# Optimization experiments

Hardware: AMD Instinct MI355X
Metric: run time of the kernel (lower is better)

The kernel has to match this reference:

```python
import jax, jax.numpy as jnp
import numpy as np

EPS = 1e-8

@jax.custom_vjp
def spike(x):
    # Heaviside forward, SuperSpike surrogate gradient in backward
    return (x > 0.0).astype(x.dtype)

def _spike_fwd(x):
    return spike(x), x

def _spike_bwd(x, g):
    return (g / (1.0 + 10.0 * jnp.abs(x)) ** 2,)

spike.defvjp(_spike_fwd, _spike_bwd)


def setup_inputs() -> dict:
    key = jax.random.key(0)
    k1, k2, k3, k4 = jax.random.split(key, 4)
    B, T, I, O = 128, 128, 1024, 1024
    x = jax.random.normal(k1, (B, T, I), dtype=jnp.float32)
    # w ~ N(0, 1/sqrt(I)) per reset_parameters
    w = jax.random.normal(k2, (I, O), dtype=jnp.float32) * np.float32(1.0 / np.sqrt(I))
    # beta ~ N(0.7, 0.01), clamped to [0,1]
    beta = jnp.clip(0.7 + 0.01 * jax.random.normal(k3, (1,), dtype=jnp.float32), 0.0, 1.0)
    # b ~ N(1.0, 0.01), clamped to >= 0
    b = jnp.clip(1.0 + 0.01 * jax.random.normal(k4, (1024,), dtype=jnp.float32), 0.0, None)
    return {"x": x, "w": w, "beta": beta, "b": b}


def reference(x, w, beta, b):
    # x: [B, T, I]; w: [I, O]; beta: [1]; b: [O]
    h = jnp.einsum('btc,cd->btd', x, w)                 # [B, T, O]
    d = jnp.einsum('ab,ac->bc', w, w)                    # lateral reset matrix [O, O]
    norm = (w ** 2).sum(0)                               # [O]
    inv_norm = 1.0 / (norm + EPS)
    B, O = x.shape[0], w.shape[1]

    def step(carry, h_t):
        mem, spk = carry
        rst = spk @ d                                    # [B, O]
        mem = (mem - rst) * beta + h_t * (1.0 - beta)
        mthr = mem * inv_norm - b
        spk = spike(mthr)
        return (mem, spk), spk

    init = (jnp.zeros((B, O), x.dtype), jnp.zeros((B, O), x.dtype))
    _, spk_rec = jax.lax.scan(step, init, jnp.swapaxes(h, 0, 1))  # [T, B, O]
    spk_rec = jnp.swapaxes(spk_rec, 0, 1)                # [B, T, O]
    loss = 0.5 * (spk_rec ** 2).mean()
    return spk_rec, loss
```

## Files before the change

kernel.cpp:

```cpp
#include <hip/hip_runtime.h>

#define B_ 128
#define T_ 128
#define I_ 1024
#define O_ 1024
#define M_ (B_*T_)
#define NOUT (M_*O_)

typedef __attribute__((ext_vector_type(8))) short short8;
typedef __attribute__((ext_vector_type(4))) float floatx4;

__device__ __forceinline__ void gld_lds16(const void* g, void* l) {
    __builtin_amdgcn_global_load_lds((const __attribute__((address_space(1))) void*)g,
                                     (__attribute__((address_space(3))) void*)l,
                                     16, 0, 0);
}

__device__ __forceinline__ void barrier_lds_only() {
    asm volatile("" ::: "memory");
    __builtin_amdgcn_s_waitcnt(0xC07F);
    __builtin_amdgcn_s_barrier();
    asm volatile("" ::: "memory");
}

__device__ __forceinline__ void split3(float x, unsigned short& h,
                                       unsigned short& m, unsigned short& l) {
    unsigned int b0 = __float_as_uint(x);
    h = (unsigned short)(b0 >> 16);
    float r1 = x - __uint_as_float(b0 & 0xFFFF0000u);
    unsigned int b1 = __float_as_uint(r1);
    m = (unsigned short)(b1 >> 16);
    float r2 = r1 - __uint_as_float(b1 & 0xFFFF0000u);
    l = (unsigned short)(__float_as_uint(r2) >> 16);
}

__global__ __launch_bounds__(256) void split_x(const float* __restrict__ X,
                                               unsigned short* __restrict__ Xh,
                                               unsigned short* __restrict__ Xm,
                                               unsigned short* __restrict__ Xl) {
    size_t base = ((size_t)blockIdx.x * 256 + threadIdx.x) * 4;
    float4 v = *(const float4*)(X + base);
    ushort4 hh, mm, ll;
    split3(v.x, hh.x, mm.x, ll.x);
    split3(v.y, hh.y, mm.y, ll.y);
    split3(v.z, hh.z, mm.z, ll.z);
    split3(v.w, hh.w, mm.w, ll.w);
    *(ushort4*)(Xh + base) = hh;
    *(ushort4*)(Xm + base) = mm;
    *(ushort4*)(Xl + base) = ll;
}

__global__ __launch_bounds__(256) void split_wt(const float* __restrict__ W,
                                                unsigned short* __restrict__ WTh,
                                                unsigned short* __restrict__ WTm,
                                                unsigned short* __restrict__ WTl) {
    __shared__ float t[64][65];
    const int tid = threadIdx.x;
    const int tx = tid & 63, ty4 = tid >> 6;
    const int r0 = blockIdx.x * 64, c0 = blockIdx.y * 64;
#pragma unroll
    for (int j = 0; j < 16; ++j) {
        int row = j * 4 + ty4;
        t[row][tx] = W[(size_t)(r0 + row) * O_ + c0 + tx];
    }
    __syncthreads();
#pragma unroll
    for (int j = 0; j < 16; ++j) {
        int i = j * 4 + ty4;
        float v = t[tx][i];
        unsigned short h, m, l;
        split3(v, h, m, l);
        size_t off = (size_t)(c0 + i) * I_ + r0 + tx;
        WTh[off] = h; WTm[off] = m; WTl[off] = l;
    }
}

__global__ __launch_bounds__(256, 3) void gemm_h_mfma(
        const unsigned short* __restrict__ Xh, const unsigned short* __restrict__ Xm,
        const unsigned short* __restrict__ Xl, const unsigned short* __restrict__ WTh,
        const unsigned short* __restrict__ WTm, const unsigned short* __restrict__ WTl,
        float* __restrict__ H) {
    const int K = I_, N = O_;
    __shared__ unsigned short P[6][128 * 32];

    const int tid = threadIdx.x;
    const int lane = tid & 63;
    const int wid = tid >> 6;
    const int wrow = wid >> 1, wcol = wid & 1;
    const int l15 = lane & 15, quad = lane >> 4;
    const int bm = blockIdx.x * 128, bn = blockIdx.y * 128;

    const int srow = tid >> 2, sch = tid & 3;
    const int schg = sch ^ ((srow >> 1) & 3);
    const unsigned short* gsrc[6];
    gsrc[0] = Xh  + (size_t)(bm + srow) * K + schg * 8;
    gsrc[1] = Xm  + (size_t)(bm + srow) * K + schg * 8;
    gsrc[2] = Xl  + (size_t)(bm + srow) * K + schg * 8;
    gsrc[3] = WTh + (size_t)(bn + srow) * K + schg * 8;
    gsrc[4] = WTm + (size_t)(bn + srow) * K + schg * 8;
    gsrc[5] = WTl + (size_t)(bn + srow) * K + schg * 8;

    floatx4 acc[4][4];
#pragma unroll
    for (int mt = 0; mt < 4; ++mt)
#pragma unroll
        for (int nt = 0; nt < 4; ++nt) acc[mt][nt] = (floatx4)(0.f);

    for (int kt = 0; kt < 32; ++kt) {
        const int k0 = kt * 32;
        __syncthreads();
#pragma unroll
        for (int p = 0; p < 6; ++p) {
            unsigned short* dst = (unsigned short*)P + p * 4096 + tid * 8;
            gld_lds16(gsrc[p] + k0, dst);
            gld_lds16(gsrc[p] + (size_t)64 * K + k0, dst + 2048);
        }
        __syncthreads();

        short8 Af[3][4];
#pragma unroll
        for (int pa = 0; pa < 3; ++pa)
#pragma unroll
            for (int mt = 0; mt < 4; ++mt) {
                int row = wrow * 64 + mt * 16 + l15;
                int chk = quad ^ ((row >> 1) & 3);
                Af[pa][mt] = *(const short8*)((const unsigned short*)P + pa * 4096 + row * 32 + chk * 8);
            }
#pragma unroll
        for (int pb = 0; pb < 3; ++pb) {
            short8 Bf[4];
#pragma unroll
            for (int nt = 0; nt < 4; ++nt) {
                int col = wcol * 64 + nt * 16 + l15;
                int chk = quad ^ ((col >> 1) & 3);
                Bf[nt] = *(const short8*)((const unsigned short*)P + (3 + pb) * 4096 + col * 32 + chk * 8);
            }
#pragma unroll
            for (int nt = 0; nt < 4; ++nt)
#pragma unroll
                for (int mt = 0; mt < 4; ++mt) {
                    acc[mt][nt] = __builtin_amdgcn_mfma_f32_16x16x32_bf16(Af[0][mt], Bf[nt], acc[mt][nt], 0, 0, 0);
                    acc[mt][nt] = __builtin_amdgcn_mfma_f32_16x16x32_bf16(Af[1][mt], Bf[nt], acc[mt][nt], 0, 0, 0);
                    if (pb < 2)
                        acc[mt][nt] = __builtin_amdgcn_mfma_f32_16x16x32_bf16(Af[2][mt], Bf[nt], acc[mt][nt], 0, 0, 0);
                }
        }
    }

#pragma unroll
    for (int mt = 0; mt < 4; ++mt)
#pragma unroll
        for (int nt = 0; nt < 4; ++nt) {
            int grow = bm + wrow * 64 + mt * 16 + quad * 4;
            int gcol = bn + wcol * 64 + nt * 16 + l15;
            float* hp = H + (size_t)grow * N + gcol;
#pragma unroll
            for (int r = 0; r < 4; ++r) hp[(size_t)r * N] = acc[mt][nt][r];
        }
}

__global__ __launch_bounds__(256) void gemm_wtw(const float* __restrict__ W,
                                                float* __restrict__ D) {
    const int K = I_, N = O_;
    __shared__ float As[32][68];
    __shared__ float Bs[32][68];
    const int tid = threadIdx.x;
    const int tx = tid & 15, ty = tid >> 4;
    const int bj = blockIdx.x * 64, bo = blockIdx.y * 64;
    const int lr = tid >> 4;
    const int lc = (tid & 15) << 2;

    float acc[4][4];
#pragma unroll
    for (int m = 0; m < 4; m++)
#pragma unroll
        for (int n = 0; n < 4; n++) acc[m][n] = 0.f;

    for (int k0 = 0; k0 < K; k0 += 32) {
        float4 a0 = *(const float4*)(W + (size_t)(k0 + lr) * N + bj + lc);
        float4 a1 = *(const float4*)(W + (size_t)(k0 + lr + 16) * N + bj + lc);
        float4 b0 = *(const float4*)(W + (size_t)(k0 + lr) * N + bo + lc);
        float4 b1 = *(const float4*)(W + (size_t)(k0 + lr + 16) * N + bo + lc);
        __syncthreads();
        *(float4*)&As[lr][lc] = a0; *(float4*)&As[lr + 16][lc] = a1;
        *(float4*)&Bs[lr][lc] = b0; *(float4*)&Bs[lr + 16][lc] = b1;
        __syncthreads();
#pragma unroll
        for (int k = 0; k < 32; ++k) {
            float4 av = *(const float4*)&As[k][ty * 4];
            float4 bv = *(const float4*)&Bs[k][tx * 4];
            float am[4] = {av.x, av.y, av.z, av.w};
            float bb[4] = {bv.x, bv.y, bv.z, bv.w};
#pragma unroll
            for (int m = 0; m < 4; m++)
#pragma unroll
                for (int n = 0; n < 4; n++) acc[m][n] += am[m] * bb[n];
        }
    }
#pragma unroll
    for (int m = 0; m < 4; m++) {
        float4 v = make_float4(acc[m][0], acc[m][1], acc[m][2], acc[m][3]);
        *(float4*)(D + (size_t)(bj + ty * 4 + m) * N + bo + tx * 4) = v;
    }
}

__global__ void colnorm_diag(const float* __restrict__ D, float* __restrict__ invn,
                             unsigned int* __restrict__ counter) {
    int o = blockIdx.x * 256 + threadIdx.x;
    if (o == 0) *counter = 0u;
    invn[o] = 1.0f / (D[(size_t)o * O_ + o] + 1e-8f);
}

__global__ __launch_bounds__(256) void scan_kernel(const float* __restrict__ h,
                                                   const float* __restrict__ d,
                                                   const float* __restrict__ invn,
                                                   const float* __restrict__ bias,
                                                   const float* __restrict__ beta,
                                                   float* __restrict__ out,
                                                   unsigned int* __restrict__ spike_count) {
    __shared__ int lst[2][O_];
    __shared__ int cnt[T_ + 1];
    __shared__ unsigned int red[256];

    const int tid = threadIdx.x;
    const int lane = tid & 63;
    const int b = blockIdx.x;
    const int o4 = tid * 4;
    const float betav = beta[0];
    const float omb = 1.0f - betav;

    const float4 invn4 = *(const float4*)(invn + o4);
    const float4 b4 = *(const float4*)(bias + o4);
    float4 mem4 = make_float4(0.f, 0.f, 0.f, 0.f);

    for (int i = tid; i <= T_; i += 256) cnt[i] = 0;
    unsigned int local_count = 0;
    const float* hb = h + (size_t)b * T_ * O_;
    float* ob = out + (size_t)b * T_ * O_;
    const unsigned long long below = (lane == 63) ? 0xFFFFFFFFFFFFFFFFull >> 1
                                                  : ((1ull << lane) - 1ull);

    float4 hcur = *(const float4*)(hb + o4);
    __syncthreads();

    for (int t = 0; t < T_; ++t) {
        const int p = t & 1, q = p ^ 1;
        const int n = cnt[t];

        float4 hnext = make_float4(0.f, 0.f, 0.f, 0.f);
        if (t + 1 < T_) hnext = *(const float4*)(hb + (size_t)(t + 1) * O_ + o4);

        float4 rst = make_float4(0.f, 0.f, 0.f, 0.f);
        int i = 0;
        for (; i + 16 <= n; i += 16) {
            float4 v[16];
#pragma unroll
            for (int u = 0; u < 16; ++u) {
                const int j = lst[p][i + u];
                v[u] = *(const float4*)(d + (size_t)j * O_ + o4);
            }
#pragma unroll
            for (int u = 0; u < 16; ++u) {
                rst.x += v[u].x; rst.y += v[u].y;
                rst.z += v[u].z; rst.w += v[u].w;
            }
        }
        for (; i + 4 <= n; i += 4) {
            float4 v[4];
#pragma unroll
            for (int u = 0; u < 4; ++u) {
                const int j = lst[p][i + u];
                v[u] = *(const float4*)(d + (size_t)j * O_ + o4);
            }
#pragma unroll
            for (int u = 0; u < 4; ++u) {
                rst.x += v[u].x; rst.y += v[u].y;
                rst.z += v[u].z; rst.w += v[u].w;
            }
        }
        for (; i < n; ++i) {
            const int j = lst[p][i];
            float4 v = *(const float4*)(d + (size_t)j * O_ + o4);
            rst.x += v.x; rst.y += v.y; rst.z += v.z; rst.w += v.w;
        }

        mem4.x = (mem4.x - rst.x) * betav + hcur.x * omb;
        mem4.y = (mem4.y - rst.y) * betav + hcur.y * omb;
        mem4.z = (mem4.z - rst.z) * betav + hcur.z * omb;
        mem4.w = (mem4.w - rst.w) * betav + hcur.w * omb;

        const int s[4] = {(mem4.x * invn4.x - b4.x) > 0.0f,
                          (mem4.y * invn4.y - b4.y) > 0.0f,
                          (mem4.z * invn4.z - b4.z) > 0.0f,
                          (mem4.w * invn4.w - b4.w) > 0.0f};

        float4 sv = make_float4(s[0] ? 1.f : 0.f, s[1] ? 1.f : 0.f,
                                s[2] ? 1.f : 0.f, s[3] ? 1.f : 0.f);
        *(float4*)(ob + (size_t)t * O_ + o4) = sv;
        local_count += (unsigned)(s[0] + s[1] + s[2] + s[3]);

#pragma unroll
        for (int u = 0; u < 4; ++u) {
            unsigned long long mask = __ballot(s[u]);
            int base = 0;
            if (lane == 0 && mask) base = atomicAdd(&cnt[t + 1], __popcll(mask));
            base = __shfl(base, 0, 64);
            if (s[u]) lst[q][base + __popcll(mask & below)] = o4 + u;
        }

        barrier_lds_only();
        hcur = hnext;
    }

    red[tid] = local_count;
    __syncthreads();
    for (int st = 128; st > 0; st >>= 1) {
        if (tid < st) red[tid] += red[tid + st];
        __syncthreads();
    }
    if (tid == 0) atomicAdd(spike_count, red[0]);
}

__global__ void finalize_loss(const unsigned int* __restrict__ spike_count,
                              float* __restrict__ loss_out) {
    *loss_out = 0.5f * ((float)(*spike_count) / 16777216.0f);
}

extern "C" void kernel_launch(void* const* d_in, const int* in_sizes, int n_in,
                              void* d_out, int out_size, void* d_ws, size_t ws_size,
                              hipStream_t stream) {
    const float* x    = (const float*)d_in[0];
    const float* w    = (const float*)d_in[1];
    const float* beta = (const float*)d_in[2];
    const float* bias = (const float*)d_in[3];
    float* out = (float*)d_out;

    char* ws = (char*)d_ws;
    float* h    = (float*)ws;
    float* dmat = (float*)(ws + (size_t)67108864);
    float* invn = (float*)(ws + (size_t)71303168);
    unsigned int* cntp = (unsigned int*)(ws + (size_t)71307264);
    unsigned short* wt_h = (unsigned short*)(ws + (size_t)71311360);
    unsigned short* wt_m = (unsigned short*)(ws + (size_t)73408512);
    unsigned short* wt_l = (unsigned short*)(ws + (size_t)75505664);
    unsigned short* x_h  = (unsigned short*)(ws + (size_t)77602816);
    unsigned short* x_m  = (unsigned short*)(ws + (size_t)111157248);
    unsigned short* x_l  = (unsigned short*)(ws + (size_t)144711680);

    split_x<<<M_ * I_ / 1024, 256, 0, stream>>>(x, x_h, x_m, x_l);
    split_wt<<<dim3(I_ / 64, O_ / 64), 256, 0, stream>>>(w, wt_h, wt_m, wt_l);
    gemm_h_mfma<<<dim3(M_ / 128, O_ / 128), 256, 0, stream>>>(x_h, x_m, x_l,
                                                              wt_h, wt_m, wt_l, h);
    gemm_wtw<<<dim3(O_ / 64, O_ / 64), 256, 0, stream>>>(w, dmat);
    colnorm_diag<<<O_ / 256, 256, 0, stream>>>(dmat, invn, cntp);
    scan_kernel<<<B_, 256, 0, stream>>>(h, dmat, invn, bias, beta, out, cntp);
    finalize_loss<<<1, 1, 0, stream>>>(cntp, out + (size_t)NOUT);
}
```

Measured before the change: 539.9 us.

## Switch split-GEMM to fp16 triple split with fewer MFMA terms; batch spike-list atomics

The three-way split of x and W moves from bf16 to fp16. fp16's longer mantissa lets the h GEMM drop cross terms, going from 8 to 6 MFMAs per k-step while aiming to keep near-fp32 accuracy. fp16 has a narrower exponent range, so small residuals may underflow; this is presumably acceptable for these input magnitudes. Separately, the spike-list append in the recurrence now does one atomicAdd per wave per timestep instead of four, using prefix offsets from the four ballots.

Result: faster. 489.0 us (-9.4%).

```diff
diff --git a/kernel.cpp b/kernel.cpp
--- a/kernel.cpp
+++ b/kernel.cpp
@@ -1,4 +1,5 @@
 #include <hip/hip_runtime.h>
+#include <hip/hip_fp16.h>
 
 #define B_ 128
 #define T_ 128
@@ -7,7 +8,7 @@
 #define M_ (B_*T_)
 #define NOUT (M_*O_)
 
-typedef __attribute__((ext_vector_type(8))) short short8;
+typedef __attribute__((ext_vector_type(8))) _Float16 half8;
 typedef __attribute__((ext_vector_type(4))) float floatx4;
 
 __device__ __forceinline__ void gld_lds16(const void* g, void* l) {
@@ -23,15 +24,16 @@
     asm volatile("" ::: "memory");
 }
 
-__device__ __forceinline__ void split3(float x, unsigned short& h,
-                                       unsigned short& m, unsigned short& l) {
-    unsigned int b0 = __float_as_uint(x);
-    h = (unsigned short)(b0 >> 16);
-    float r1 = x - __uint_as_float(b0 & 0xFFFF0000u);
-    unsigned int b1 = __float_as_uint(r1);
-    m = (unsigned short)(b1 >> 16);
-    float r2 = r1 - __uint_as_float(b1 & 0xFFFF0000u);
-    l = (unsigned short)(__float_as_uint(r2) >> 16);
+__device__ __forceinline__ void split3h(float x, unsigned short& h,
+                                        unsigned short& m, unsigned short& l) {
+    __half f0 = __float2half(x);
+    float r1 = x - __half2float(f0);
+    __half f1 = __float2half(r1);
+    float r2 = r1 - __half2float(f1);
+    __half f2 = __float2half(r2);
+    h = __half_as_ushort(f0);
+    m = __half_as_ushort(f1);
+    l = __half_as_ushort(f2);
 }
 
 __global__ __launch_bounds__(256) void split_x(const float* __restrict__ X,
@@ -41,10 +43,10 @@
     size_t base = ((size_t)blockIdx.x * 256 + threadIdx.x) * 4;
     float4 v = *(const float4*)(X + base);
     ushort4 hh, mm, ll;
-    split3(v.x, hh.x, mm.x, ll.x);
-    split3(v.y, hh.y, mm.y, ll.y);
-    split3(v.z, hh.z, mm.z, ll.z);
-    split3(v.w, hh.w, mm.w, ll.w);
+    split3h(v.x, hh.x, mm.x, ll.x);
+    split3h(v.y, hh.y, mm.y, ll.y);
+    split3h(v.z, hh.z, mm.z, ll.z);
+    split3h(v.w, hh.w, mm.w, ll.w);
     *(ushort4*)(Xh + base) = hh;
     *(ushort4*)(Xm + base) = mm;
     *(ushort4*)(Xl + base) = ll;
@@ -69,7 +71,7 @@
         int i = j * 4 + ty4;
         float v = t[tx][i];
         unsigned short h, m, l;
-        split3(v, h, m, l);
+        split3h(v, h, m, l);
         size_t off = (size_t)(c0 + i) * I_ + r0 + tx;
         WTh[off] = h; WTm[off] = m; WTl[off] = l;
     }
@@ -117,32 +119,33 @@
         }
         __syncthreads();
 
-        short8 Af[3][4];
+        half8 Af[3][4];
 #pragma unroll
         for (int pa = 0; pa < 3; ++pa)
 #pragma unroll
             for (int mt = 0; mt < 4; ++mt) {
                 int row = wrow * 64 + mt * 16 + l15;
                 int chk = quad ^ ((row >> 1) & 3);
-                Af[pa][mt] = *(const short8*)((const unsigned short*)P + pa * 4096 + row * 32 + chk * 8);
+                Af[pa][mt] = *(const half8*)((const unsigned short*)P + pa * 4096 + row * 32 + chk * 8);
             }
 #pragma unroll
         for (int pb = 0; pb < 3; ++pb) {
-            short8 Bf[4];
+            half8 Bf[4];
 #pragma unroll
             for (int nt = 0; nt < 4; ++nt) {
                 int col = wcol * 64 + nt * 16 + l15;
                 int chk = quad ^ ((col >> 1) & 3);
-                Bf[nt] = *(const short8*)((const unsigned short*)P + (3 + pb) * 4096 + col * 32 + chk * 8);
+                Bf[nt] = *(const half8*)((const unsigned short*)P + (3 + pb) * 4096 + col * 32 + chk * 8);
             }
 #pragma unroll
             for (int nt = 0; nt < 4; ++nt)
 #pragma unroll
                 for (int mt = 0; mt < 4; ++mt) {
-                    acc[mt][nt] = __builtin_amdgcn_mfma_f32_16x16x32_bf16(Af[0][mt], Bf[nt], acc[mt][nt], 0, 0, 0);
-                    acc[mt][nt] = __builtin_amdgcn_mfma_f32_16x16x32_bf16(Af[1][mt], Bf[nt], acc[mt][nt], 0, 0, 0);
+                    acc[mt][nt] = __builtin_amdgcn_mfma_f32_16x16x32_f16(Af[0][mt], Bf[nt], acc[mt][nt], 0, 0, 0);
                     if (pb < 2)
-                        acc[mt][nt] = __builtin_amdgcn_mfma_f32_16x16x32_bf16(Af[2][mt], Bf[nt], acc[mt][nt], 0, 0, 0);
+                        acc[mt][nt] = __builtin_amdgcn_mfma_f32_16x16x32_f16(Af[1][mt], Bf[nt], acc[mt][nt], 0, 0, 0);
+                    if (pb == 0)
+                        acc[mt][nt] = __builtin_amdgcn_mfma_f32_16x16x32_f16(Af[2][mt], Bf[nt], acc[mt][nt], 0, 0, 0);
                 }
         }
     }
@@ -299,14 +302,22 @@
         *(float4*)(ob + (size_t)t * O_ + o4) = sv;
         local_count += (unsigned)(s[0] + s[1] + s[2] + s[3]);
 
-#pragma unroll
-        for (int u = 0; u < 4; ++u) {
-            unsigned long long mask = __ballot(s[u]);
-            int base = 0;
-            if (lane == 0 && mask) base = atomicAdd(&cnt[t + 1], __popcll(mask));
-            base = __shfl(base, 0, 64);
-            if (s[u]) lst[q][base + __popcll(mask & below)] = o4 + u;
-        }
+        unsigned long long mk0 = __ballot(s[0]);
+        unsigned long long mk1 = __ballot(s[1]);
+        unsigned long long mk2 = __ballot(s[2]);
+        unsigned long long mk3 = __ballot(s[3]);
+        const int c0 = __popcll(mk0), c1 = __popcll(mk1), c2 = __popcll(mk2);
+        const int tot = c0 + c1 + c2 + __popcll(mk3);
+        int base = 0;
+        if (lane == 0 && tot) base = atomicAdd(&cnt[t + 1], tot);
+        base = __shfl(base, 0, 64);
+        if (s[0]) lst[q][base + __popcll(mk0 & below)] = o4 + 0;
+        base += c0;
+        if (s[1]) lst[q][base + __popcll(mk1 & below)] = o4 + 1;
+        base += c1;
+        if (s[2]) lst[q][base + __popcll(mk2 & below)] = o4 + 2;
+        base += c2;
+        if (s[3]) lst[q][base + __popcll(mk3 & below)] = o4 + 3;
 
         barrier_lds_only();
         hcur = hnext;
```
